# Optimization experiments

Hardware: AMD Instinct MI355X
Metric: run time of the kernel (lower is better)

## Reference

```python
import jax, jax.numpy as jnp
import numpy as np

DISCRETIZATION = "IM"  # matches init_kwargs


def setup_inputs() -> dict:
    key = jax.random.key(0)
    ks = jax.random.split(key, 6)
    Bt, L, H, P = 16, 4096, 128, 256
    std = 1.0 / np.sqrt(H)
    return {
        "inputs": jax.random.normal(ks[0], (Bt, L, H), jnp.float32),
        "A_diag": jax.random.uniform(ks[1], (P,), jnp.float32, 0.0, 1.0),
        "B": jax.random.uniform(ks[2], (P, H, 2), jnp.float32, -std, std),
        "C": jax.random.uniform(ks[3], (H, P, 2), jnp.float32, -std, std),
        "D": jax.random.normal(ks[4], (H,), jnp.float32),
        "steps": jax.random.uniform(ks[5], (P,), jnp.float32, 0.0, 1.0),
    }


def _combine(l, r):
    # 2x2 block composition: new_A = r.A @ l.A ; new_b = r.A @ l.b + r.b
    la11, la12, la21, la22, lb1, lb2 = l
    ra11, ra12, ra21, ra22, rb1, rb2 = r
    c11 = ra11 * la11 + ra12 * la21
    c12 = ra11 * la12 + ra12 * la22
    c21 = ra21 * la11 + ra22 * la21
    c22 = ra21 * la12 + ra22 * la22
    nb1 = ra11 * lb1 + ra12 * lb2 + rb1
    nb2 = ra21 * lb1 + ra22 * lb2 + rb2
    return (c11, c12, c21, c22, nb1, nb2)


def reference(inputs, A_diag, B, C, D, steps):
    Bt, L, H = inputs.shape
    P = A_diag.shape[0]
    a = jax.nn.relu(A_diag)                 # (P,)
    step = jax.nn.sigmoid(steps)            # (P,)
    Bc = jax.lax.complex(B[..., 0], B[..., 1])   # (P, H) complex64
    Cc = jax.lax.complex(C[..., 0], C[..., 1])   # (H, P) complex64

    # bu = inputs @ B^T  -> (Bt, L, P), complex
    bu = jnp.einsum("blh,ph->blp", inputs.astype(jnp.complex64), Bc)

    if DISCRETIZATION == "IM":
        s2a = step * step * a
        schur = 1.0 / (1.0 + s2a)
        m11 = 1.0 - s2a * schur
        m12 = -step * a * schur
        m21 = step * schur
        m22 = schur
        f1 = (m11 * step) * bu
        f2 = (m21 * step) * bu
    else:  # IMEX
        m11 = jnp.ones_like(a)
        m12 = -step * a
        m21 = step
        m22 = 1.0 - step * step * a
        f1 = bu * step
        f2 = bu * (step * step)

    # sequence axis leading for the scan: (L, Bt, P)
    f1 = jnp.moveaxis(f1, 1, 0)
    f2 = jnp.moveaxis(f2, 1, 0)
    # time-invariant 2x2 per-channel blocks, broadcast to (L, 1, P) complex
    a_elems = tuple(
        jnp.broadcast_to(m.astype(jnp.complex64)[None, None, :], (L, 1, P))
        for m in (m11, m12, m21, m22)
    )
    _, _, _, _, _x1, x2 = jax.lax.associative_scan(
        _combine, (*a_elems, f1, f2), axis=0
    )
    states = x2  # (L, Bt, P): position component (index 1 of 2x2 state)

    projected = jnp.einsum("lbp,hp->blh", states, Cc).real  # (Bt, L, H)
    return projected + inputs * D
```

## Files before the change

kernel.cpp:

```cpp
#include <hip/hip_runtime.h>
#include <math.h>


constexpr int BTc = 16;
constexpr int Lc  = 4096;
constexpr int Hc  = 128;
constexpr int Pc  = 256;
constexpr int CL  = 64;
constexpr int NC  = Lc / CL;
constexpr int LOG2CL = 6;

typedef __attribute__((ext_vector_type(8))) short short8;
typedef __attribute__((ext_vector_type(4))) float f32x4;

constexpr size_t CF_OFF  = 0;
constexpr size_t BF_OFF  = 16384;
constexpr size_t CFR_OFF = BF_OFF + 131072;
constexpr size_t LOC_OFF = CFR_OFF + 131072;
constexpr size_t INI_OFF = LOC_OFF + 4194304;

constexpr int LDS_U  = 0;
constexpr int LDS_BU = 16384;
constexpr int LDS_XS = 82944;
constexpr int LDS_BYTES = 115712;

__device__ __forceinline__ unsigned short f2bf(float x) {
    unsigned u = __float_as_uint(x);
    u += 0x7fffu + ((u >> 16) & 1u);
    return (unsigned short)(u >> 16);
}
__device__ __forceinline__ float bf2f(unsigned short h) {
    return __uint_as_float(((unsigned)h) << 16);
}
__device__ __forceinline__ f32x4 mfma16(short8 a, short8 b, f32x4 c) {
    return __builtin_amdgcn_mfma_f32_16x16x32_bf16(a, b, c, 0, 0, 0);
}

__global__ __launch_bounds__(256) void k_prep(const float* __restrict__ A_diag,
                                              const float* __restrict__ steps,
                                              const float* __restrict__ Bw,
                                              const float* __restrict__ Cw,
                                              float* __restrict__ cf,
                                              unsigned short* __restrict__ BF,
                                              unsigned short* __restrict__ CFr) {
    int idx = blockIdx.x * 256 + threadIdx.x;
    {
        int j = idx & 7, lane = (idx >> 3) & 63, nfg = (idx >> 9) & 31, kt = idx >> 14;
        int k = kt * 32 + (lane >> 4) * 8 + j;
        int n = nfg * 16 + (lane & 15);
        int p = n >> 1, part = n & 1;
        BF[idx] = f2bf(Bw[(p * Hc + k) * 2 + part]);
    }
    {
        int j = idx & 7, lane = (idx >> 3) & 63, nfg = (idx >> 9) & 7, ktG = idx >> 12;
        int k = ktG * 32 + (lane >> 4) * 8 + j;
        int h = nfg * 16 + (lane & 15);
        int p = k >> 1, part = k & 1;
        float v = Cw[(h * Pc + p) * 2 + part];
        CFr[idx] = f2bf(part ? -v : v);
    }
    if (blockIdx.x == 0) {
        int p = threadIdx.x;
        float a  = fmaxf(A_diag[p], 0.0f);
        float st = 1.0f / (1.0f + expf(-steps[p]));
        float s2a   = st * st * a;
        float schur = 1.0f / (1.0f + s2a);
        float m11 = 1.0f - s2a * schur;
        float m12 = -st * a * schur;
        float m21 = st * schur;
        float m22 = schur;
        cf[0*Pc+p] = m11;  cf[1*Pc+p] = m12;
        cf[2*Pc+p] = m21;  cf[3*Pc+p] = m22;
        cf[4*Pc+p] = m11 * st;
        cf[5*Pc+p] = m21 * st;
        float a11=m11, a12=m12, a21=m21, a22=m22;
        #pragma unroll
        for (int i = 0; i < LOG2CL; i++) {
            float b11 = a11*a11 + a12*a21;
            float b12 = a11*a12 + a12*a22;
            float b21 = a21*a11 + a22*a21;
            float b22 = a21*a12 + a22*a22;
            a11=b11; a12=b12; a21=b21; a22=b22;
        }
        cf[6*Pc+p]=a11; cf[7*Pc+p]=a12; cf[8*Pc+p]=a21; cf[9*Pc+p]=a22;
    }
}

__global__ __launch_bounds__(512) void k_scanB(const float* __restrict__ cf,
                                               const float2* __restrict__ loc,
                                               float2* __restrict__ ini) {
    int b = blockIdx.x, n = threadIdx.x;
    int p = n >> 1;
    float A11=cf[6*Pc+p], A12=cf[7*Pc+p], A21=cf[8*Pc+p], A22=cf[9*Pc+p];
    float x1 = 0.f, x2 = 0.f;
    for (int c = 0; c < NC; c++) {
        size_t idx = ((size_t)(b * NC + c)) * 512 + n;
        ini[idx] = make_float2(x1, x2);
        float2 lv = loc[idx];
        float n1 = fmaf(A11, x1, fmaf(A12, x2, lv.x));
        float n2 = fmaf(A21, x1, fmaf(A22, x2, lv.y));
        x1 = n1; x2 = n2;
    }
}

template<int PASS>
__global__ __launch_bounds__(512, 2) void k_pass(const float* __restrict__ in,
                                                 const float* __restrict__ cf,
                                                 const unsigned short* __restrict__ BF,
                                                 const unsigned short* __restrict__ CFr,
                                                 const float* __restrict__ Dw,
                                                 float2* __restrict__ loc,
                                                 const float2* __restrict__ ini,
                                                 float* __restrict__ out) {
    __shared__ float4 smem4[LDS_BYTES / 16];
    char* sm = (char*)smem4;
    float* BU = (float*)(sm + LDS_BU);

    int tid  = threadIdx.x;
    int lane = tid & 63;
    int w    = tid >> 6;
    int wm   = w >> 2, wn = w & 3;
    int bc   = blockIdx.x;
    size_t mbase = (size_t)bc * CL;

    {
        int l   = tid >> 3;
        int kc0 = (tid & 7) * 2;
        const float* g = in + (mbase + l) * Hc + (tid & 7) * 16;
        float4 f0 = *(const float4*)(g);
        float4 f1 = *(const float4*)(g + 4);
        float4 f2 = *(const float4*)(g + 8);
        float4 f3 = *(const float4*)(g + 12);
        short8 c0, c1;
        c0[0]=(short)f2bf(f0.x); c0[1]=(short)f2bf(f0.y); c0[2]=(short)f2bf(f0.z); c0[3]=(short)f2bf(f0.w);
        c0[4]=(short)f2bf(f1.x); c0[5]=(short)f2bf(f1.y); c0[6]=(short)f2bf(f1.z); c0[7]=(short)f2bf(f1.w);
        c1[0]=(short)f2bf(f2.x); c1[1]=(short)f2bf(f2.y); c1[2]=(short)f2bf(f2.z); c1[3]=(short)f2bf(f2.w);
        c1[4]=(short)f2bf(f3.x); c1[5]=(short)f2bf(f3.y); c1[6]=(short)f2bf(f3.z); c1[7]=(short)f2bf(f3.w);
        int sw = l & 7;
        *(short8*)(sm + LDS_U + l * 256 + (((kc0    ) ^ sw) << 4)) = c0;
        *(short8*)(sm + LDS_U + l * 256 + (((kc0 + 1) ^ sw) << 4)) = c1;
    }
    __syncthreads();

    f32x4 acc2[2][2];
    if constexpr (PASS == 2) {
        #pragma unroll
        for (int i = 0; i < 2; i++)
            #pragma unroll
            for (int j = 0; j < 2; j++) acc2[i][j] = (f32x4)(0.0f);
    }

    for (int half = 0; half < 2; ++half) {
        f32x4 acc[2][4];
        #pragma unroll
        for (int i = 0; i < 2; i++)
            #pragma unroll
            for (int j = 0; j < 4; j++) acc[i][j] = (f32x4)(0.0f);

        int r = lane & 15, q = lane >> 4;
        #pragma unroll
        for (int kt = 0; kt < 4; ++kt) {
            short8 a[2];
            #pragma unroll
            for (int mf = 0; mf < 2; ++mf) {
                int la = wm * 32 + mf * 16 + r;
                int kc = kt * 4 + q;
                a[mf] = *(const short8*)(sm + LDS_U + la * 256 + ((kc ^ (la & 7)) << 4));
            }
            #pragma unroll
            for (int nfi = 0; nfi < 4; ++nfi) {
                int nfg = half * 16 + wn * 4 + nfi;
                short8 bb = *(const short8*)(BF + (size_t)((kt * 32 + nfg) * 64 + lane) * 8);
                acc[0][nfi] = mfma16(a[0], bb, acc[0][nfi]);
                acc[1][nfi] = mfma16(a[1], bb, acc[1][nfi]);
            }
        }

        __syncthreads();
        #pragma unroll
        for (int mf = 0; mf < 2; ++mf)
            #pragma unroll
            for (int nfi = 0; nfi < 4; ++nfi)
                #pragma unroll
                for (int j = 0; j < 4; ++j) {
                    int l  = wm * 32 + mf * 16 + (lane >> 4) * 4 + j;
                    int nn = wn * 64 + nfi * 16 + (lane & 15);
                    BU[l * 260 + nn] = acc[mf][nfi][j];
                }
        __syncthreads();

        if (tid < 256) {
            int n = tid, ng = half * 256 + n, p = ng >> 1;
            float m11 = cf[p],        m12 = cf[256 + p];
            float m21 = cf[512 + p],  m22 = cf[768 + p];
            float s1  = cf[1024 + p], s2  = cf[1280 + p];
            float x1, x2;
            if constexpr (PASS == 1) { x1 = 0.f; x2 = 0.f; }
            else { float2 iv = ini[(size_t)bc * 512 + ng]; x1 = iv.x; x2 = iv.y; }
            if constexpr (PASS == 1) {
                #pragma unroll 4
                for (int l = 0; l < CL; ++l) {
                    float f  = BU[l * 260 + n];
                    float n1 = fmaf(m11, x1, fmaf(m12, x2, s1 * f));
                    float n2 = fmaf(m21, x1, fmaf(m22, x2, s2 * f));
                    x1 = n1; x2 = n2;
                }
                loc[(size_t)bc * 512 + ng] = make_float2(x1, x2);
            } else {
                unsigned kc = n >> 3, e = n & 7;
                #pragma unroll 4
                for (int l = 0; l < CL; ++l) {
                    float f  = BU[l * 260 + n];
                    float n1 = fmaf(m11, x1, fmaf(m12, x2, s1 * f));
                    float n2 = fmaf(m21, x1, fmaf(m22, x2, s2 * f));
                    x1 = n1; x2 = n2;
                    *(unsigned short*)(sm + LDS_XS + l * 512 + ((kc ^ (unsigned)(l & 7)) << 4) + e * 2)
                        = f2bf(x2);
                }
            }
        }

        if constexpr (PASS == 2) {
            __syncthreads();
            #pragma unroll
            for (int kt = 0; kt < 8; ++kt) {
                short8 a2[2];
                #pragma unroll
                for (int mf = 0; mf < 2; ++mf) {
                    int la  = wm * 32 + mf * 16 + r;
                    int kc2 = kt * 4 + q;
                    a2[mf] = *(const short8*)(sm + LDS_XS + la * 512 + ((kc2 ^ (la & 7)) << 4));
                }
                #pragma unroll
                for (int nfi = 0; nfi < 2; ++nfi) {
                    int ktG = half * 8 + kt;
                    int nfg = wn * 2 + nfi;
                    short8 bb = *(const short8*)(CFr + (size_t)((ktG * 8 + nfg) * 64 + lane) * 8);
                    acc2[0][nfi] = mfma16(a2[0], bb, acc2[0][nfi]);
                    acc2[1][nfi] = mfma16(a2[1], bb, acc2[1][nfi]);
                }
            }
            __syncthreads();
        }
    }

    if constexpr (PASS == 2) {
        #pragma unroll
        for (int nfi = 0; nfi < 2; ++nfi) {
            int h = wn * 32 + nfi * 16 + (lane & 15);
            float d = Dw[h];
            #pragma unroll
            for (int mf = 0; mf < 2; ++mf)
                #pragma unroll
                for (int j = 0; j < 4; ++j) {
                    int l = wm * 32 + mf * 16 + (lane >> 4) * 4 + j;
                    size_t gm = mbase + l;
                    out[gm * Hc + h] = acc2[mf][nfi][j] + in[gm * Hc + h] * d;
                }
        }
    }
}

extern "C" void kernel_launch(void* const* d_in, const int* in_sizes, int n_in,
                              void* d_out, int out_size, void* d_ws, size_t ws_size,
                              hipStream_t stream) {
    const float* in  = (const float*)d_in[0];
    const float* Ad  = (const float*)d_in[1];
    const float* Bw  = (const float*)d_in[2];
    const float* Cw  = (const float*)d_in[3];
    const float* Dw  = (const float*)d_in[4];
    const float* stp = (const float*)d_in[5];
    char* ws = (char*)d_ws;
    float*          cf  = (float*)(ws + CF_OFF);
    unsigned short* BF  = (unsigned short*)(ws + BF_OFF);
    unsigned short* CFr = (unsigned short*)(ws + CFR_OFF);
    float2*         loc = (float2*)(ws + LOC_OFF);
    float2*         ini = (float2*)(ws + INI_OFF);
    float* out = (float*)d_out;

    k_prep<<<256, 256, 0, stream>>>(Ad, stp, Bw, Cw, cf, BF, CFr);
    k_pass<1><<<BTc * NC, 512, 0, stream>>>(in, cf, BF, CFr, Dw, loc, ini, out);
    k_scanB<<<BTc, 512, 0, stream>>>(cf, loc, ini);
    k_pass<2><<<BTc * NC, 512, 0, stream>>>(in, cf, BF, CFr, Dw, loc, ini, out);
}
```

Baseline: 171.9 us.

## Run chunk scan on all 512 threads with bf16 in-place LDS buffer

The k_pass kernel now computes both column halves of the input projection first and stores them as bf16 in a swizzled LDS buffer. All 512 threads then run the per-channel recurrence at once, where before only 256 threads ran it per half. In pass 2 the states are written back in place and fed to the output MFMA, and the separate fp32 BU and XS buffers are dropped. The smaller LDS footprint allows launch_bounds(512,4) for higher occupancy, and the k_scanB loads are batched in groups of 8. In exchange, the scan input is rounded to bf16, which adds error before the recurrence.

```diff
diff --git a/kernel.cpp b/kernel.cpp
--- a/kernel.cpp
+++ b/kernel.cpp
@@ -19,10 +19,9 @@
 constexpr size_t LOC_OFF = CFR_OFF + 131072;
 constexpr size_t INI_OFF = LOC_OFF + 4194304;
 
-constexpr int LDS_U  = 0;
-constexpr int LDS_BU = 16384;
-constexpr int LDS_XS = 82944;
-constexpr int LDS_BYTES = 115712;
+constexpr int LDS_U   = 0;
+constexpr int LDS_BUX = 16384;
+constexpr int LDS_BYTES = 81920;
 
 __device__ __forceinline__ unsigned short f2bf(float x) {
     unsigned u = __float_as_uint(x);
@@ -35,6 +34,7 @@
 __device__ __forceinline__ f32x4 mfma16(short8 a, short8 b, f32x4 c) {
     return __builtin_amdgcn_mfma_f32_16x16x32_bf16(a, b, c, 0, 0, 0);
 }
+__device__ __forceinline__ int swz(int l) { return (l ^ (l >> 3)) & 7; }
 
 __global__ __launch_bounds__(256) void k_prep(const float* __restrict__ A_diag,
                                               const float* __restrict__ steps,
@@ -93,18 +93,24 @@
     int p = n >> 1;
     float A11=cf[6*Pc+p], A12=cf[7*Pc+p], A21=cf[8*Pc+p], A22=cf[9*Pc+p];
     float x1 = 0.f, x2 = 0.f;
-    for (int c = 0; c < NC; c++) {
-        size_t idx = ((size_t)(b * NC + c)) * 512 + n;
-        ini[idx] = make_float2(x1, x2);
-        float2 lv = loc[idx];
-        float n1 = fmaf(A11, x1, fmaf(A12, x2, lv.x));
-        float n2 = fmaf(A21, x1, fmaf(A22, x2, lv.y));
-        x1 = n1; x2 = n2;
+    for (int g = 0; g < 8; g++) {
+        float2 lv[8];
+        #pragma unroll
+        for (int j = 0; j < 8; j++)
+            lv[j] = loc[((size_t)(b * NC + g * 8 + j)) * 512 + n];
+        #pragma unroll
+        for (int j = 0; j < 8; j++) {
+            size_t idx = ((size_t)(b * NC + g * 8 + j)) * 512 + n;
+            ini[idx] = make_float2(x1, x2);
+            float n1 = fmaf(A11, x1, fmaf(A12, x2, lv[j].x));
+            float n2 = fmaf(A21, x1, fmaf(A22, x2, lv[j].y));
+            x1 = n1; x2 = n2;
+        }
     }
 }
 
 template<int PASS>
-__global__ __launch_bounds__(512, 2) void k_pass(const float* __restrict__ in,
+__global__ __launch_bounds__(512, 4) void k_pass(const float* __restrict__ in,
                                                  const float* __restrict__ cf,
                                                  const unsigned short* __restrict__ BF,
                                                  const unsigned short* __restrict__ CFr,
@@ -114,7 +120,6 @@
                                                  float* __restrict__ out) {
     __shared__ float4 smem4[LDS_BYTES / 16];
     char* sm = (char*)smem4;
-    float* BU = (float*)(sm + LDS_BU);
 
     int tid  = threadIdx.x;
     int lane = tid & 63;
@@ -122,6 +127,7 @@
     int wm   = w >> 2, wn = w & 3;
     int bc   = blockIdx.x;
     size_t mbase = (size_t)bc * CL;
+    int r = lane & 15, q = lane >> 4;
 
     {
         int l   = tid >> 3;
@@ -142,14 +148,7 @@
     }
     __syncthreads();
 
-    f32x4 acc2[2][2];
-    if constexpr (PASS == 2) {
-        #pragma unroll
-        for (int i = 0; i < 2; i++)
-            #pragma unroll
-            for (int j = 0; j < 2; j++) acc2[i][j] = (f32x4)(0.0f);
-    }
-
+    #pragma unroll
     for (int half = 0; half < 2; ++half) {
         f32x4 acc[2][4];
         #pragma unroll
@@ -157,7 +156,6 @@
             #pragma unroll
             for (int j = 0; j < 4; j++) acc[i][j] = (f32x4)(0.0f);
 
-        int r = lane & 15, q = lane >> 4;
         #pragma unroll
         for (int kt = 0; kt < 4; ++kt) {
             short8 a[2];
@@ -175,53 +173,56 @@
                 acc[1][nfi] = mfma16(a[1], bb, acc[1][nfi]);
             }
         }
-
+        char* bux = sm + LDS_BUX + half * 32768;
+        #pragma unroll
+        for (int mf = 0; mf < 2; ++mf)
+            #pragma unroll
+            for (int nfi = 0; nfi < 4; ++nfi) {
+                int nn = wn * 64 + nfi * 16 + r;
+                int kc = nn >> 3, e = nn & 7;
+                #pragma unroll
+                for (int j = 0; j < 4; ++j) {
+                    int l = wm * 32 + mf * 16 + q * 4 + j;
+                    *(unsigned short*)(bux + l * 512 + ((kc ^ swz(l)) << 4) + e * 2)
+                        = f2bf(acc[mf][nfi][j]);
+                }
+            }
+    }
+    __syncthreads();
+
+    {
+        int ng = tid, h = ng >> 8, n = ng & 255, p = ng >> 1;
+        float m11 = cf[p],        m12 = cf[256 + p];
+        float m21 = cf[512 + p],  m22 = cf[768 + p];
+        float s1  = cf[1024 + p], s2  = cf[1280 + p];
+        float x1, x2;
+        if constexpr (PASS == 1) { x1 = 0.f; x2 = 0.f; }
+        else { float2 iv = ini[(size_t)bc * 512 + ng]; x1 = iv.x; x2 = iv.y; }
+        char* bux = sm + LDS_BUX + h * 32768 + (n & 7) * 2;
+        int kc = n >> 3;
+        #pragma unroll 4
+        for (int l = 0; l < CL; ++l) {
+            char* addr = bux + l * 512 + ((kc ^ swz(l)) << 4);
+            float f  = bf2f(*(unsigned short*)addr);
+            float n1 = fmaf(m11, x1, fmaf(m12, x2, s1 * f));
+            float n2 = fmaf(m21, x1, fmaf(m22, x2, s2 * f));
+            x1 = n1; x2 = n2;
+            if constexpr (PASS == 2) *(unsigned short*)addr = f2bf(x2);
+        }
+        if constexpr (PASS == 1) loc[(size_t)bc * 512 + ng] = make_float2(x1, x2);
+    }
+
+    if constexpr (PASS == 2) {
         __syncthreads();
-        #pragma unroll
-        for (int mf = 0; mf < 2; ++mf)
-            #pragma unroll
-            for (int nfi = 0; nfi < 4; ++nfi)
-                #pragma unroll
-                for (int j = 0; j < 4; ++j) {
-                    int l  = wm * 32 + mf * 16 + (lane >> 4) * 4 + j;
-                    int nn = wn * 64 + nfi * 16 + (lane & 15);
-                    BU[l * 260 + nn] = acc[mf][nfi][j];
-                }
-        __syncthreads();
-
-        if (tid < 256) {
-            int n = tid, ng = half * 256 + n, p = ng >> 1;
-            float m11 = cf[p],        m12 = cf[256 + p];
-            float m21 = cf[512 + p],  m22 = cf[768 + p];
-            float s1  = cf[1024 + p], s2  = cf[1280 + p];
-            float x1, x2;
-            if constexpr (PASS == 1) { x1 = 0.f; x2 = 0.f; }
-            else { float2 iv = ini[(size_t)bc * 512 + ng]; x1 = iv.x; x2 = iv.y; }
-            if constexpr (PASS == 1) {
-                #pragma unroll 4
-                for (int l = 0; l < CL; ++l) {
-                    float f  = BU[l * 260 + n];
-                    float n1 = fmaf(m11, x1, fmaf(m12, x2, s1 * f));
-                    float n2 = fmaf(m21, x1, fmaf(m22, x2, s2 * f));
-                    x1 = n1; x2 = n2;
-                }
-                loc[(size_t)bc * 512 + ng] = make_float2(x1, x2);
-            } else {
-                unsigned kc = n >> 3, e = n & 7;
-                #pragma unroll 4
-                for (int l = 0; l < CL; ++l) {
-                    float f  = BU[l * 260 + n];
-                    float n1 = fmaf(m11, x1, fmaf(m12, x2, s1 * f));
-                    float n2 = fmaf(m21, x1, fmaf(m22, x2, s2 * f));
-                    x1 = n1; x2 = n2;
-                    *(unsigned short*)(sm + LDS_XS + l * 512 + ((kc ^ (unsigned)(l & 7)) << 4) + e * 2)
-                        = f2bf(x2);
-                }
-            }
-        }
-
-        if constexpr (PASS == 2) {
-            __syncthreads();
+        f32x4 acc2[2][2];
+        #pragma unroll
+        for (int i = 0; i < 2; i++)
+            #pragma unroll
+            for (int j = 0; j < 2; j++) acc2[i][j] = (f32x4)(0.0f);
+
+        #pragma unroll
+        for (int half = 0; half < 2; ++half) {
+            char* bux = sm + LDS_BUX + half * 32768;
             #pragma unroll
             for (int kt = 0; kt < 8; ++kt) {
                 short8 a2[2];
@@ -229,7 +230,7 @@
                 for (int mf = 0; mf < 2; ++mf) {
                     int la  = wm * 32 + mf * 16 + r;
                     int kc2 = kt * 4 + q;
-                    a2[mf] = *(const short8*)(sm + LDS_XS + la * 512 + ((kc2 ^ (la & 7)) << 4));
+                    a2[mf] = *(const short8*)(bux + la * 512 + ((kc2 ^ swz(la)) << 4));
                 }
                 #pragma unroll
                 for (int nfi = 0; nfi < 2; ++nfi) {
@@ -240,22 +241,18 @@
                     acc2[1][nfi] = mfma16(a2[1], bb, acc2[1][nfi]);
                 }
             }
-            __syncthreads();
-        }
-    }
-
-    if constexpr (PASS == 2) {
+        }
         #pragma unroll
         for (int nfi = 0; nfi < 2; ++nfi) {
-            int h = wn * 32 + nfi * 16 + (lane & 15);
+            int h = wn * 32 + nfi * 16 + r;
             float d = Dw[h];
             #pragma unroll
             for (int mf = 0; mf < 2; ++mf)
                 #pragma unroll
                 for (int j = 0; j < 4; ++j) {
-                    int l = wm * 32 + mf * 16 + (lane >> 4) * 4 + j;
+                    int l = wm * 32 + mf * 16 + q * 4 + j;
                     size_t gm = mbase + l;
-                    out[gm * Hc + h] = acc2[mf][nfi][j] + in[gm * Hc + h] * d;
+                    out[gm * Hc + h] = fmaf(in[gm * Hc + h], d, acc2[mf][nfi][j]);
                 }
         }
     }
```

New measurement: 150.9 us. 12.2% less time.
